# Kernel tuning notes

Hardware: AMD Instinct MI355X
Metric: run time of the kernel (lower is better)

The kernel has to match this reference:

```python
import jax, jax.numpy as jnp
import numpy as np

H, DH = 8, 64          # heads, dim_head
SCALE = DH ** -0.5

def _ln(x, g, b, eps=1e-5):
    m = jnp.mean(x, axis=-1, keepdims=True)
    v = jnp.var(x, axis=-1, keepdims=True)
    return (x - m) / jnp.sqrt(v + eps) * g + b

def setup_inputs() -> dict:
    key = jax.random.key(0)
    ks = jax.random.split(key, 16)
    b, n, din, dim, depth, mlp, nc = 4, 2048, 768, 512, 2, 512, 2
    s = 0.02
    x = jax.random.normal(ks[0], (b, n, din), jnp.float32)
    lens = jax.random.randint(ks[1], (b,), n // 2, n + 1)
    lens = lens.at[0].set(n)  # ensure amax(lens) == n so torch's truncation is a no-op
    return {
        "x": x,
        "lens": lens,
        "cls_token": jax.random.normal(ks[2], (1, 1, dim), jnp.float32),
        "fc_w": jax.random.normal(ks[3], (din, dim), jnp.float32) * s,
        "fc_b": jnp.zeros((dim,), jnp.float32),
        "ln1_g": jnp.ones((depth, dim), jnp.float32),
        "ln1_b": jnp.zeros((depth, dim), jnp.float32),
        "qkv_w": jax.random.normal(ks[4], (depth, dim, 3 * H * DH), jnp.float32) * s,
        "out_w": jax.random.normal(ks[5], (depth, H * DH, dim), jnp.float32) * s,
        "out_b": jnp.zeros((depth, dim), jnp.float32),
        "ln2_g": jnp.ones((depth, dim), jnp.float32),
        "ln2_b": jnp.zeros((depth, dim), jnp.float32),
        "ff1_w": jax.random.normal(ks[6], (depth, dim, mlp), jnp.float32) * s,
        "ff1_b": jnp.zeros((depth, mlp), jnp.float32),
        "ff2_w": jax.random.normal(ks[7], (depth, mlp, dim), jnp.float32) * s,
        "ff2_b": jnp.zeros((depth, dim), jnp.float32),
        "lnf_g": jnp.ones((dim,), jnp.float32),
        "lnf_b": jnp.zeros((dim,), jnp.float32),
        "head_w": jax.random.normal(ks[8], (dim, nc), jnp.float32) * s,
        "head_b": jnp.zeros((nc,), jnp.float32),
    }

def reference(x, lens, cls_token, fc_w, fc_b, ln1_g, ln1_b, qkv_w, out_w, out_b,
              ln2_g, ln2_b, ff1_w, ff1_b, ff2_w, ff2_b, lnf_g, lnf_b, head_w, head_b):
    b, n, _ = x.shape
    # fc + GELU (exact erf gelu, matching torch nn.GELU default)
    x = jax.nn.gelu(x @ fc_w + fc_b, approximate=False)
    x = jnp.concatenate([jnp.broadcast_to(cls_token, (b, 1, x.shape[-1])), x], axis=1)
    n1 = n + 1
    lens1 = lens + 1
    # faithful mask: mask @ mask.mT -> True only where BOTH query and key are padding
    pad = jnp.arange(n1)[None, :] >= lens1[:, None]           # [b, n1]
    mask2 = pad[:, :, None] & pad[:, None, :]                  # [b, n1, n1]
    neg = -jnp.finfo(x.dtype).max
    depth = qkv_w.shape[0]
    for l in range(depth):
        xn = _ln(x, ln1_g[l], ln1_b[l])
        qkv = xn @ qkv_w[l]                                    # [b, n1, 3*H*DH]
        q, k, v = jnp.split(qkv, 3, axis=-1)
        q = q.reshape(b, n1, H, DH).transpose(0, 2, 1, 3)      # [b, h, n1, dh]
        k = k.reshape(b, n1, H, DH).transpose(0, 2, 1, 3)
        v = v.reshape(b, n1, H, DH).transpose(0, 2, 1, 3)
        dots = jnp.einsum('bhid,bhjd->bhij', q, k) * SCALE
        dots = jnp.where(mask2[:, None], neg, dots)
        dots = dots - jnp.max(dots, axis=-1, keepdims=True)
        attn = jax.nn.softmax(dots, axis=-1)
        o = jnp.einsum('bhij,bhjd->bhid', attn, v)
        o = o.transpose(0, 2, 1, 3).reshape(b, n1, H * DH)
        x = o @ out_w[l] + out_b[l] + x
        h = jax.nn.gelu(_ln(x, ln2_g[l], ln2_b[l]) @ ff1_w[l] + ff1_b[l], approximate=False)
        x = h @ ff2_w[l] + ff2_b[l] + x
    x = _ln(x, lnf_g, lnf_b)
    return x[:, 0] @ head_w + head_b   # pool='cls'
```

## Files before the change

kernel.cpp:

```cpp
#include <hip/hip_runtime.h>
#include <hip/hip_bf16.h>
#include <math.h>
#include <float.h>

typedef __hip_bfloat16 bf16;
using bf16x8 = __attribute__((ext_vector_type(8))) __bf16;
using f32x4  = __attribute__((ext_vector_type(4))) float;

constexpr int BATCH = 4;
constexpr int SEQ   = 2048;
constexpr int SEQ1  = 2049;
constexpr int DIN   = 768;
constexpr int DIMC  = 512;
constexpr int DEPTH = 2;
constexpr int NHEAD = 8;
constexpr int DHEAD = 64;
constexpr int ROWS  = BATCH * SEQ1;
constexpr int VKP   = 2112;
constexpr float ATT_SCALE = 0.125f;
constexpr float NEGBIG = -1e30f;

__device__ __forceinline__ bf16x8 ld_frag(const bf16* p) { return *(const bf16x8*)p; }

__device__ __forceinline__ void g2lds16(const bf16* g, bf16* l) {
    __builtin_amdgcn_global_load_lds(
        (const __attribute__((address_space(1))) void*)g,
        (__attribute__((address_space(3))) void*)l, 16, 0, 0);
}

__global__ __launch_bounds__(256) void cast_kernel(const float* __restrict__ src,
                                                   bf16* __restrict__ dst, int n4) {
    int i = blockIdx.x * 256 + threadIdx.x;
    if (i < n4) {
        float4 v = ((const float4*)src)[i];
        dst[i * 4 + 0] = __float2bfloat16(v.x);
        dst[i * 4 + 1] = __float2bfloat16(v.y);
        dst[i * 4 + 2] = __float2bfloat16(v.z);
        dst[i * 4 + 3] = __float2bfloat16(v.w);
    }
}

__global__ __launch_bounds__(256) void wt_transpose_kernel(
    const float* __restrict__ src, bf16* __restrict__ dst,
    int R, int C, long zstride) {
    __shared__ bf16 tile[32][33];
    int z = blockIdx.z;
    const float* s = src + (size_t)z * zstride;
    bf16* d = dst + (size_t)z * zstride;
    int tx = threadIdx.x, ty = threadIdx.y;
    int c0 = blockIdx.x * 32, r0 = blockIdx.y * 32;
    int c = c0 + tx;
#pragma unroll
    for (int rr = ty; rr < 32; rr += 8) {
        int r = r0 + rr;
        tile[rr][tx] = (r < R && c < C) ? __float2bfloat16(s[(size_t)r * C + c])
                                        : __float2bfloat16(0.f);
    }
    __syncthreads();
    int rc = r0 + tx;
#pragma unroll
    for (int cc = ty; cc < 32; cc += 8) {
        int oc = c0 + cc;
        if (rc < R && oc < C) d[(size_t)oc * R + rc] = tile[tx][cc];
    }
}

__global__ __launch_bounds__(256) void vt_transpose_kernel(
    const bf16* __restrict__ QKV, bf16* __restrict__ VT) {
    __shared__ bf16 tile[32][33];
    int z = blockIdx.z;
    int bb = z >> 3, hh = z & 7;
    const bf16* s = QKV + (size_t)bb * SEQ1 * 1536 + 1024 + hh * 64;
    bf16* d = VT + (size_t)z * 64 * VKP;
    int tx = threadIdx.x, ty = threadIdx.y;
    int c0 = blockIdx.x * 32, r0 = blockIdx.y * 32;
    int c = c0 + tx;
#pragma unroll
    for (int rr = ty; rr < 32; rr += 8) {
        int r = r0 + rr;
        tile[rr][tx] = (r < SEQ1) ? s[(size_t)r * 1536 + c] : __float2bfloat16(0.f);
    }
    __syncthreads();
    int rc = r0 + tx;
#pragma unroll
    for (int cc = ty; cc < 32; cc += 8) {
        int oc = c0 + cc;
        if (rc < VKP) d[(size_t)oc * VKP + rc] = tile[tx][cc];
    }
}

__global__ void cls_fill_kernel(const float* __restrict__ cls, float* __restrict__ X) {
    int b = blockIdx.x;
    for (int d = threadIdx.x; d < DIMC; d += blockDim.x)
        X[(size_t)b * SEQ1 * DIMC + d] = cls[d];
}

template<int BM, bool GELU_, bool RESID, bool REMAP, bool OBF>
__global__ __launch_bounds__(256) void gemm_bt(
    const bf16* __restrict__ A, const bf16* __restrict__ Bt,
    const float* __restrict__ bias, const float* __restrict__ resid,
    float* __restrict__ Cf, bf16* __restrict__ Ch, int M, int N, int K) {
    constexpr int MI = BM / 32;
    __shared__ __align__(16) bf16 As[BM * 32];
    __shared__ __align__(16) bf16 Bs[4096];
    int tid = threadIdx.x;
    int ln = tid & 63, wv = tid >> 6;
    int wr = wv >> 1, wc = wv & 1;
    int l15 = ln & 15, l4 = ln >> 4;
    int m0 = blockIdx.y * BM, n0 = blockIdx.x * 128;

    f32x4 acc[MI][4];
#pragma unroll
    for (int i = 0; i < MI; ++i)
#pragma unroll
        for (int j = 0; j < 4; ++j) acc[i][j] = {0.f, 0.f, 0.f, 0.f};

    int aslot[MI], bslot[4];
#pragma unroll
    for (int i = 0; i < MI; ++i) {
        int m = wr * (BM / 2) + i * 16 + l15;
        aslot[i] = m * 4 + (l4 ^ ((m >> 1) & 3));
    }
#pragma unroll
    for (int j = 0; j < 4; ++j) {
        int n = wc * 64 + j * 16 + l15;
        bslot[j] = n * 4 + (l4 ^ ((n >> 1) & 3));
    }

    for (int k0 = 0; k0 < K; k0 += 32) {
#pragma unroll
        for (int r = 0; r < BM / 64; ++r) {
            int s = r * 256 + tid;
            int m = s >> 2, c = s & 3;
            int kb = c ^ ((m >> 1) & 3);
            int gm = m0 + m; if (gm > M - 1) gm = M - 1;
            g2lds16(A + (size_t)gm * K + k0 + kb * 8, &As[s * 8]);
        }
#pragma unroll
        for (int r = 0; r < 2; ++r) {
            int s = r * 256 + tid;
            int n = s >> 2, c = s & 3;
            int kb = c ^ ((n >> 1) & 3);
            g2lds16(Bt + (size_t)(n0 + n) * K + k0 + kb * 8, &Bs[s * 8]);
        }
        __syncthreads();
        bf16x8 af[MI], bfr[4];
#pragma unroll
        for (int i = 0; i < MI; ++i) af[i] = ld_frag(&As[aslot[i] * 8]);
#pragma unroll
        for (int j = 0; j < 4; ++j) bfr[j] = ld_frag(&Bs[bslot[j] * 8]);
#pragma unroll
        for (int i = 0; i < MI; ++i)
#pragma unroll
            for (int j = 0; j < 4; ++j)
                acc[i][j] = __builtin_amdgcn_mfma_f32_16x16x32_bf16(af[i], bfr[j], acc[i][j], 0, 0, 0);
        __syncthreads();
    }

#pragma unroll
    for (int i = 0; i < MI; ++i) {
#pragma unroll
        for (int j = 0; j < 4; ++j) {
            int gn = n0 + wc * 64 + j * 16 + l15;
            float bb = bias ? bias[gn] : 0.f;
#pragma unroll
            for (int r = 0; r < 4; ++r) {
                int gm = m0 + wr * (BM / 2) + i * 16 + l4 * 4 + r;
                if (gm >= M) continue;
                float v = acc[i][j][r] + bb;
                if (GELU_) v = 0.5f * v * (1.f + erff(v * 0.70710678118654752f));
                size_t orow = gm;
                if (REMAP) { int b_ = gm >> 11; orow = (size_t)b_ * SEQ1 + (gm & 2047) + 1; }
                size_t oi = orow * (size_t)N + gn;
                if (RESID) v += resid[oi];
                if (OBF) Ch[oi] = __float2bfloat16(v); else Cf[oi] = v;
            }
        }
    }
}

__global__ __launch_bounds__(256) void ln_kernel(const float* __restrict__ Xin, bf16* __restrict__ Xout,
                          const float* __restrict__ g, const float* __restrict__ bb) {
    int row = blockIdx.x;
    int t = threadIdx.x;
    const float* xr = Xin + (size_t)row * DIMC;
    float v0 = xr[t], v1 = xr[t + 256];
    __shared__ float red[256];
    red[t] = v0 + v1;
    __syncthreads();
    for (int w = 128; w > 0; w >>= 1) { if (t < w) red[t] += red[t + w]; __syncthreads(); }
    float mean = red[0] * (1.f / 512.f);
    __syncthreads();
    float d0 = v0 - mean, d1 = v1 - mean;
    red[t] = d0 * d0 + d1 * d1;
    __syncthreads();
    for (int w = 128; w > 0; w >>= 1) { if (t < w) red[t] += red[t + w]; __syncthreads(); }
    float rinv = rsqrtf(red[0] * (1.f / 512.f) + 1e-5f);
    bf16* orow = Xout + (size_t)row * DIMC;
    orow[t]       = __float2bfloat16(d0 * rinv * g[t]       + bb[t]);
    orow[t + 256] = __float2bfloat16(d1 * rinv * g[t + 256] + bb[t + 256]);
}

__global__ __launch_bounds__(256, 4) void attn_kernel(
    const bf16* __restrict__ QKV, const bf16* __restrict__ VT,
    const int* __restrict__ lens, bf16* __restrict__ O) {
    constexpr int KS = 72;
    __shared__ __align__(16) bf16 Ks[2][64 * KS];
    __shared__ __align__(16) bf16 Vs[2][64 * KS];
    int tid = threadIdx.x, ln = tid & 63, wv = tid >> 6;
    int l15 = ln & 15, l4 = ln >> 4;
    int q0 = blockIdx.x * 64, h = blockIdx.y, b = blockIdx.z;
    int len1 = lens[b] + 1;
    const bf16* qkv_b = QKV + (size_t)b * SEQ1 * 1536;
    const bf16* vt_b  = VT + (size_t)(b * 8 + h) * 64 * VKP;

    uint4 z4 = make_uint4(0u, 0u, 0u, 0u);
    uint4 q0v = z4, q1v = z4;
    int qrow = q0 + wv * 16 + l15;
    if (qrow < SEQ1) {
        const bf16* qp = qkv_b + (size_t)qrow * 1536 + h * 64 + l4 * 8;
        q0v = *(const uint4*)qp;
        q1v = *(const uint4*)(qp + 32);
    }
    bf16x8 bq0 = __builtin_bit_cast(bf16x8, q0v);
    bf16x8 bq1 = __builtin_bit_cast(bf16x8, q1v);
    bool qpad = (qrow >= len1);

    float mrun = NEGBIG, lrun = 0.f;
    f32x4 oaccT[4];
#pragma unroll
    for (int t = 0; t < 4; ++t) oaccT[t] = {0.f, 0.f, 0.f, 0.f};

    uint4 kr[2], vr[2];
    int srow[2], sseg[2], krow[2];
#pragma unroll
    for (int rr = 0; rr < 2; ++rr) {
        int idx = rr * 256 + tid;
        int row = idx >> 3, seg = idx & 7;
        srow[rr] = row; sseg[rr] = seg;
        int pb = row >> 5, w = row & 31;
        krow[rr] = pb * 32 + ((w >> 2) & 1) * 16 + (w >> 3) * 4 + (w & 3);
    }

#pragma unroll
    for (int rr = 0; rr < 2; ++rr) {
        kr[rr] = (srow[rr] < SEQ1)
            ? *(const uint4*)(qkv_b + (size_t)srow[rr] * 1536 + 512 + h * 64 + sseg[rr] * 8) : z4;
        vr[rr] = *(const uint4*)(vt_b + (size_t)srow[rr] * VKP + sseg[rr] * 8);
    }
#pragma unroll
    for (int rr = 0; rr < 2; ++rr) {
        *(uint4*)&Ks[0][krow[rr] * KS + sseg[rr] * 8] = kr[rr];
        *(uint4*)&Vs[0][srow[rr] * KS + sseg[rr] * 8] = vr[rr];
    }
    __syncthreads();

    for (int kt = 0; kt < 33; ++kt) {
        int k0 = kt * 64;
        int buf = kt & 1;
        if (kt < 32) {
            int kn = k0 + 64;
#pragma unroll
            for (int rr = 0; rr < 2; ++rr) {
                kr[rr] = (kn + srow[rr] < SEQ1)
                    ? *(const uint4*)(qkv_b + (size_t)(kn + srow[rr]) * 1536 + 512 + h * 64 + sseg[rr] * 8) : z4;
                vr[rr] = *(const uint4*)(vt_b + (size_t)srow[rr] * VKP + kn + sseg[rr] * 8);
            }
        }

        f32x4 sacc[2][2];
#pragma unroll
        for (int pb = 0; pb < 2; ++pb)
#pragma unroll
            for (int s = 0; s < 2; ++s) {
                int R = pb * 32 + s * 16 + l15;
                f32x4 a = {0.f, 0.f, 0.f, 0.f};
                bf16x8 kf0 = ld_frag(&Ks[buf][R * KS + l4 * 8]);
                bf16x8 kf1 = ld_frag(&Ks[buf][R * KS + 32 + l4 * 8]);
                a = __builtin_amdgcn_mfma_f32_16x16x32_bf16(kf0, bq0, a, 0, 0, 0);
                a = __builtin_amdgcn_mfma_f32_16x16x32_bf16(kf1, bq1, a, 0, 0, 0);
                sacc[pb][s] = a;
            }

        float sv[2][2][4];
        float mx = NEGBIG;
#pragma unroll
        for (int pb = 0; pb < 2; ++pb)
#pragma unroll
            for (int s = 0; s < 2; ++s)
#pragma unroll
                for (int r = 0; r < 4; ++r) {
                    int j = k0 + pb * 32 + l4 * 8 + s * 4 + r;
                    float v = sacc[pb][s][r] * ATT_SCALE;
                    if (j >= SEQ1 || (qpad && j >= len1)) v = NEGBIG;
                    sv[pb][s][r] = v;
                    mx = fmaxf(mx, v);
                }
        mx = fmaxf(mx, __shfl_xor(mx, 16, 64));
        mx = fmaxf(mx, __shfl_xor(mx, 32, 64));
        float mnew = fmaxf(mrun, mx);
        float alpha = __expf(mrun - mnew);
        float rs = 0.f;
        unsigned short pk[2][8];
#pragma unroll
        for (int pb = 0; pb < 2; ++pb)
#pragma unroll
            for (int s = 0; s < 2; ++s)
#pragma unroll
                for (int r = 0; r < 4; ++r) {
                    float ex = sv[pb][s][r] - mnew;
                    float p = (ex < -80.f) ? 0.f : __expf(ex);
                    rs += p;
                    pk[pb][s * 4 + r] = __builtin_bit_cast(unsigned short, __float2bfloat16(p));
                }
        rs += __shfl_xor(rs, 16, 64);
        rs += __shfl_xor(rs, 32, 64);
        lrun = lrun * alpha + rs;
        mrun = mnew;
#pragma unroll
        for (int t = 0; t < 4; ++t) {
            oaccT[t][0] *= alpha; oaccT[t][1] *= alpha;
            oaccT[t][2] *= alpha; oaccT[t][3] *= alpha;
        }

#pragma unroll
        for (int pb = 0; pb < 2; ++pb) {
            union { unsigned short u[8]; bf16x8 v; } pu;
#pragma unroll
            for (int e = 0; e < 8; ++e) pu.u[e] = pk[pb][e];
            bf16x8 pf = pu.v;
#pragma unroll
            for (int t = 0; t < 4; ++t) {
                bf16x8 vf = ld_frag(&Vs[buf][(t * 16 + l15) * KS + pb * 32 + l4 * 8]);
                oaccT[t] = __builtin_amdgcn_mfma_f32_16x16x32_bf16(vf, pf, oaccT[t], 0, 0, 0);
            }
        }

        if (kt < 32) {
            int ob = buf ^ 1;
#pragma unroll
            for (int rr = 0; rr < 2; ++rr) {
                *(uint4*)&Ks[ob][krow[rr] * KS + sseg[rr] * 8] = kr[rr];
                *(uint4*)&Vs[ob][srow[rr] * KS + sseg[rr] * 8] = vr[rr];
            }
        }
        __syncthreads();
    }

    if (qrow < SEQ1) {
        float rl = (lrun > 0.f) ? 1.f / lrun : 0.f;
        bf16* orow = O + ((size_t)b * SEQ1 + qrow) * DIMC + h * 64;
#pragma unroll
        for (int t = 0; t < 4; ++t) {
            union { unsigned short u[4]; uint2 v; } ou;
#pragma unroll
            for (int r = 0; r < 4; ++r)
                ou.u[r] = __builtin_bit_cast(unsigned short, __float2bfloat16(oaccT[t][r] * rl));
            *(uint2*)&orow[t * 16 + l4 * 4] = ou.v;
        }
    }
}

__global__ __launch_bounds__(256) void head_kernel(const float* __restrict__ X,
                            const float* __restrict__ g, const float* __restrict__ bb,
                            const float* __restrict__ hw, const float* __restrict__ hb,
                            float* __restrict__ out) {
    int b = blockIdx.x, t = threadIdx.x;
    const float* xr = X + (size_t)b * SEQ1 * DIMC;
    float v0 = xr[t], v1 = xr[t + 256];
    __shared__ float red[256];
    red[t] = v0 + v1;
    __syncthreads();
    for (int w = 128; w > 0; w >>= 1) { if (t < w) red[t] += red[t + w]; __syncthreads(); }
    float mean = red[0] * (1.f / 512.f);
    __syncthreads();
    float d0 = v0 - mean, d1 = v1 - mean;
    red[t] = d0 * d0 + d1 * d1;
    __syncthreads();
    for (int w = 128; w > 0; w >>= 1) { if (t < w) red[t] += red[t + w]; __syncthreads(); }
    float rinv = rsqrtf(red[0] * (1.f / 512.f) + 1e-5f);
    __syncthreads();
    float xn0 = d0 * rinv * g[t] + bb[t];
    float xn1 = d1 * rinv * g[t + 256] + bb[t + 256];
    float p0 = xn0 * hw[t * 2]     + xn1 * hw[(t + 256) * 2];
    float p1 = xn0 * hw[t * 2 + 1] + xn1 * hw[(t + 256) * 2 + 1];
    __shared__ float r0[256], r1[256];
    r0[t] = p0; r1[t] = p1;
    __syncthreads();
    for (int w = 128; w > 0; w >>= 1) { if (t < w) { r0[t] += r0[t + w]; r1[t] += r1[t + w]; } __syncthreads(); }
    if (t == 0) {
        out[b * 2 + 0] = r0[0] + hb[0];
        out[b * 2 + 1] = r1[0] + hb[1];
    }
}

extern "C" void kernel_launch(void* const* d_in, const int* in_sizes, int n_in,
                              void* d_out, int out_size, void* d_ws, size_t ws_size,
                              hipStream_t stream) {
    const float* x      = (const float*)d_in[0];
    const int*   lens   = (const int*)d_in[1];
    const float* cls    = (const float*)d_in[2];
    const float* fc_w   = (const float*)d_in[3];
    const float* fc_b   = (const float*)d_in[4];
    const float* ln1_g  = (const float*)d_in[5];
    const float* ln1_b  = (const float*)d_in[6];
    const float* qkv_w  = (const float*)d_in[7];
    const float* out_w  = (const float*)d_in[8];
    const float* out_b  = (const float*)d_in[9];
    const float* ln2_g  = (const float*)d_in[10];
    const float* ln2_b  = (const float*)d_in[11];
    const float* ff1_w  = (const float*)d_in[12];
    const float* ff1_b  = (const float*)d_in[13];
    const float* ff2_w  = (const float*)d_in[14];
    const float* ff2_b  = (const float*)d_in[15];
    const float* lnf_g  = (const float*)d_in[16];
    const float* lnf_b  = (const float*)d_in[17];
    const float* head_w = (const float*)d_in[18];
    const float* head_b = (const float*)d_in[19];
    float* out = (float*)d_out;

    char* w = (char*)d_ws;
    float* X    = (float*)w;  w += (size_t)ROWS * DIMC * 4;
    bf16*  XNh  = (bf16*)w;   w += (size_t)ROWS * DIMC * 2;
    bf16*  QKVh = (bf16*)w;   w += (size_t)ROWS * 1536 * 2;
    bf16*  Obh  = (bf16*)w;   w += (size_t)ROWS * DIMC * 2;
    bf16*  xbf  = (bf16*)w;   w += (size_t)BATCH * SEQ * DIN * 2;
    bf16*  VT   = xbf;
    bf16*  fc_wt  = (bf16*)w;
    bf16*  qkv_wt = fc_wt  + (size_t)DIN * DIMC;
    bf16*  out_wt = qkv_wt + (size_t)2 * DIMC * 1536;
    bf16*  ff1_wt = out_wt + (size_t)2 * DIMC * DIMC;
    bf16*  ff2_wt = ff1_wt + (size_t)2 * DIMC * DIMC;
    bf16*  Hbh  = Obh;

    dim3 blk(256);
    dim3 tb(32, 8);

    cast_kernel<<<dim3((BATCH * SEQ * DIN / 4 + 255) / 256), blk, 0, stream>>>(
        x, xbf, BATCH * SEQ * DIN / 4);

    wt_transpose_kernel<<<dim3(16, 24, 1), tb, 0, stream>>>(fc_w,  fc_wt,  DIN,  DIMC, (long)DIN * DIMC);
    wt_transpose_kernel<<<dim3(48, 16, 2), tb, 0, stream>>>(qkv_w, qkv_wt, DIMC, 1536, (long)DIMC * 1536);
    wt_transpose_kernel<<<dim3(16, 16, 2), tb, 0, stream>>>(out_w, out_wt, DIMC, DIMC, (long)DIMC * DIMC);
    wt_transpose_kernel<<<dim3(16, 16, 2), tb, 0, stream>>>(ff1_w, ff1_wt, DIMC, DIMC, (long)DIMC * DIMC);
    wt_transpose_kernel<<<dim3(16, 16, 2), tb, 0, stream>>>(ff2_w, ff2_wt, DIMC, DIMC, (long)DIMC * DIMC);

    gemm_bt<64, true, false, true, false><<<dim3(4, 128), blk, 0, stream>>>(
        xbf, fc_wt, fc_b, nullptr, X, nullptr, BATCH * SEQ, DIMC, DIN);
    cls_fill_kernel<<<dim3(BATCH), blk, 0, stream>>>(cls, X);

    for (int l = 0; l < DEPTH; ++l) {
        ln_kernel<<<dim3(ROWS), blk, 0, stream>>>(X, XNh, ln1_g + l * DIMC, ln1_b + l * DIMC);
        gemm_bt<128, false, false, false, true><<<dim3(12, 65), blk, 0, stream>>>(
            XNh, qkv_wt + (size_t)l * DIMC * 1536, nullptr, nullptr, nullptr, QKVh, ROWS, 1536, DIMC);
        vt_transpose_kernel<<<dim3(2, 66, 32), tb, 0, stream>>>(QKVh, VT);
        attn_kernel<<<dim3(33, NHEAD, BATCH), blk, 0, stream>>>(QKVh, VT, lens, Obh);
        gemm_bt<64, false, true, false, false><<<dim3(4, 129), blk, 0, stream>>>(
            Obh, out_wt + (size_t)l * DIMC * DIMC, out_b + l * DIMC, X, X, nullptr, ROWS, DIMC, DIMC);
        ln_kernel<<<dim3(ROWS), blk, 0, stream>>>(X, XNh, ln2_g + l * DIMC, ln2_b + l * DIMC);
        gemm_bt<64, true, false, false, true><<<dim3(4, 129), blk, 0, stream>>>(
            XNh, ff1_wt + (size_t)l * DIMC * DIMC, ff1_b + l * DIMC, nullptr, nullptr, Hbh, ROWS, DIMC, DIMC);
        gemm_bt<64, false, true, false, false><<<dim3(4, 129), blk, 0, stream>>>(
            Hbh, ff2_wt + (size_t)l * DIMC * DIMC, ff2_b + l * DIMC, X, X, nullptr, ROWS, DIMC, DIMC);
    }
    head_kernel<<<dim3(BATCH), blk, 0, stream>>>(X, lnf_g, lnf_b, head_w, head_b, out);
}
```

Baseline: 619.4 us.

## Warp-per-row LayerNorm, XOR-swizzled attention LDS, skip unneeded masking

LayerNorm now gives each row to one 64-lane wavefront with vectorized float4 loads and shuffle reductions, replacing the block-wide shared-memory tree reduction and its many barriers. The attention kernel drops the padded LDS rows in favour of an XOR-swizzled 16-byte-slot layout for K and V. The smaller footprint allows launch bounds to rise to 5 blocks per CU. Per-element masking is also skipped for key tiles that lie entirely inside the valid length. The swizzle must stay consistent between writes and fragment reads, and the higher occupancy target may constrain registers.

```diff
diff --git a/kernel.cpp b/kernel.cpp
--- a/kernel.cpp
+++ b/kernel.cpp
@@ -181,32 +181,42 @@
 
 __global__ __launch_bounds__(256) void ln_kernel(const float* __restrict__ Xin, bf16* __restrict__ Xout,
                           const float* __restrict__ g, const float* __restrict__ bb) {
-    int row = blockIdx.x;
-    int t = threadIdx.x;
-    const float* xr = Xin + (size_t)row * DIMC;
-    float v0 = xr[t], v1 = xr[t + 256];
-    __shared__ float red[256];
-    red[t] = v0 + v1;
-    __syncthreads();
-    for (int w = 128; w > 0; w >>= 1) { if (t < w) red[t] += red[t + w]; __syncthreads(); }
-    float mean = red[0] * (1.f / 512.f);
-    __syncthreads();
-    float d0 = v0 - mean, d1 = v1 - mean;
-    red[t] = d0 * d0 + d1 * d1;
-    __syncthreads();
-    for (int w = 128; w > 0; w >>= 1) { if (t < w) red[t] += red[t + w]; __syncthreads(); }
-    float rinv = rsqrtf(red[0] * (1.f / 512.f) + 1e-5f);
-    bf16* orow = Xout + (size_t)row * DIMC;
-    orow[t]       = __float2bfloat16(d0 * rinv * g[t]       + bb[t]);
-    orow[t + 256] = __float2bfloat16(d1 * rinv * g[t + 256] + bb[t + 256]);
-}
-
-__global__ __launch_bounds__(256, 4) void attn_kernel(
+    int wv = threadIdx.x >> 6, ln = threadIdx.x & 63;
+    int row = blockIdx.x * 4 + wv;
+    if (row >= ROWS) return;
+    const float* xr = Xin + (size_t)row * DIMC + ln * 8;
+    float4 a = *(const float4*)xr;
+    float4 c = *(const float4*)(xr + 4);
+    float s = a.x + a.y + a.z + a.w + c.x + c.y + c.z + c.w;
+#pragma unroll
+    for (int off = 1; off < 64; off <<= 1) s += __shfl_xor(s, off, 64);
+    float mean = s * (1.f / 512.f);
+    float d[8] = {a.x - mean, a.y - mean, a.z - mean, a.w - mean,
+                  c.x - mean, c.y - mean, c.z - mean, c.w - mean};
+    float var = 0.f;
+#pragma unroll
+    for (int e = 0; e < 8; ++e) var += d[e] * d[e];
+#pragma unroll
+    for (int off = 1; off < 64; off <<= 1) var += __shfl_xor(var, off, 64);
+    float rinv = rsqrtf(var * (1.f / 512.f) + 1e-5f);
+    const float* gp = g + ln * 8;
+    const float* bp = bb + ln * 8;
+    float4 g0 = *(const float4*)gp, g1 = *(const float4*)(gp + 4);
+    float4 b0 = *(const float4*)bp, b1 = *(const float4*)(bp + 4);
+    float gg[8] = {g0.x, g0.y, g0.z, g0.w, g1.x, g1.y, g1.z, g1.w};
+    float bbv[8] = {b0.x, b0.y, b0.z, b0.w, b1.x, b1.y, b1.z, b1.w};
+    union { unsigned short u[8]; uint4 v; } ou;
+#pragma unroll
+    for (int e = 0; e < 8; ++e)
+        ou.u[e] = __builtin_bit_cast(unsigned short, __float2bfloat16(d[e] * rinv * gg[e] + bbv[e]));
+    *(uint4*)(Xout + (size_t)row * DIMC + ln * 8) = ou.v;
+}
+
+__global__ __launch_bounds__(256, 5) void attn_kernel(
     const bf16* __restrict__ QKV, const bf16* __restrict__ VT,
     const int* __restrict__ lens, bf16* __restrict__ O) {
-    constexpr int KS = 72;
-    __shared__ __align__(16) bf16 Ks[2][64 * KS];
-    __shared__ __align__(16) bf16 Vs[2][64 * KS];
+    __shared__ __align__(16) bf16 Ks[2][4096];
+    __shared__ __align__(16) bf16 Vs[2][4096];
     int tid = threadIdx.x, ln = tid & 63, wv = tid >> 6;
     int l15 = ln & 15, l4 = ln >> 4;
     int q0 = blockIdx.x * 64, h = blockIdx.y, b = blockIdx.z;
@@ -232,14 +242,17 @@
     for (int t = 0; t < 4; ++t) oaccT[t] = {0.f, 0.f, 0.f, 0.f};
 
     uint4 kr[2], vr[2];
-    int srow[2], sseg[2], krow[2];
+    int srow[2], sseg[2];
+    int kslot[2], vslot[2];
 #pragma unroll
     for (int rr = 0; rr < 2; ++rr) {
         int idx = rr * 256 + tid;
         int row = idx >> 3, seg = idx & 7;
         srow[rr] = row; sseg[rr] = seg;
         int pb = row >> 5, w = row & 31;
-        krow[rr] = pb * 32 + ((w >> 2) & 1) * 16 + (w >> 3) * 4 + (w & 3);
+        int krow = pb * 32 + ((w >> 2) & 1) * 16 + (w >> 3) * 4 + (w & 3);
+        kslot[rr] = krow * 8 + (seg ^ (krow & 7));
+        vslot[rr] = row * 8 + (seg ^ (row & 7));
     }
 
 #pragma unroll
@@ -250,8 +263,8 @@
     }
 #pragma unroll
     for (int rr = 0; rr < 2; ++rr) {
-        *(uint4*)&Ks[0][krow[rr] * KS + sseg[rr] * 8] = kr[rr];
-        *(uint4*)&Vs[0][srow[rr] * KS + sseg[rr] * 8] = vr[rr];
+        *(uint4*)&Ks[0][kslot[rr] * 8] = kr[rr];
+        *(uint4*)&Vs[0][vslot[rr] * 8] = vr[rr];
     }
     __syncthreads();
 
@@ -275,13 +288,14 @@
             for (int s = 0; s < 2; ++s) {
                 int R = pb * 32 + s * 16 + l15;
                 f32x4 a = {0.f, 0.f, 0.f, 0.f};
-                bf16x8 kf0 = ld_frag(&Ks[buf][R * KS + l4 * 8]);
-                bf16x8 kf1 = ld_frag(&Ks[buf][R * KS + 32 + l4 * 8]);
+                bf16x8 kf0 = ld_frag(&Ks[buf][(R * 8 + (l4 ^ (R & 7))) * 8]);
+                bf16x8 kf1 = ld_frag(&Ks[buf][(R * 8 + ((l4 + 4) ^ (R & 7))) * 8]);
                 a = __builtin_amdgcn_mfma_f32_16x16x32_bf16(kf0, bq0, a, 0, 0, 0);
                 a = __builtin_amdgcn_mfma_f32_16x16x32_bf16(kf1, bq1, a, 0, 0, 0);
                 sacc[pb][s] = a;
             }
 
+        bool needmask = (k0 + 64 > len1) || (kt == 32);
         float sv[2][2][4];
         float mx = NEGBIG;
 #pragma unroll
@@ -290,9 +304,11 @@
             for (int s = 0; s < 2; ++s)
 #pragma unroll
                 for (int r = 0; r < 4; ++r) {
-                    int j = k0 + pb * 32 + l4 * 8 + s * 4 + r;
                     float v = sacc[pb][s][r] * ATT_SCALE;
-                    if (j >= SEQ1 || (qpad && j >= len1)) v = NEGBIG;
+                    if (needmask) {
+                        int j = k0 + pb * 32 + l4 * 8 + s * 4 + r;
+                        if (j >= SEQ1 || (qpad && j >= len1)) v = NEGBIG;
+                    }
                     sv[pb][s][r] = v;
                     mx = fmaxf(mx, v);
                 }
@@ -331,7 +347,8 @@
             bf16x8 pf = pu.v;
 #pragma unroll
             for (int t = 0; t < 4; ++t) {
-                bf16x8 vf = ld_frag(&Vs[buf][(t * 16 + l15) * KS + pb * 32 + l4 * 8]);
+                int VR = t * 16 + l15;
+                bf16x8 vf = ld_frag(&Vs[buf][(VR * 8 + ((pb * 4 + l4) ^ (VR & 7))) * 8]);
                 oaccT[t] = __builtin_amdgcn_mfma_f32_16x16x32_bf16(vf, pf, oaccT[t], 0, 0, 0);
             }
         }
@@ -340,8 +357,8 @@
             int ob = buf ^ 1;
 #pragma unroll
             for (int rr = 0; rr < 2; ++rr) {
-                *(uint4*)&Ks[ob][krow[rr] * KS + sseg[rr] * 8] = kr[rr];
-                *(uint4*)&Vs[ob][srow[rr] * KS + sseg[rr] * 8] = vr[rr];
+                *(uint4*)&Ks[ob][kslot[rr] * 8] = kr[rr];
+                *(uint4*)&Vs[ob][vslot[rr] * 8] = vr[rr];
             }
         }
         __syncthreads();
@@ -450,14 +467,14 @@
     cls_fill_kernel<<<dim3(BATCH), blk, 0, stream>>>(cls, X);
 
     for (int l = 0; l < DEPTH; ++l) {
-        ln_kernel<<<dim3(ROWS), blk, 0, stream>>>(X, XNh, ln1_g + l * DIMC, ln1_b + l * DIMC);
+        ln_kernel<<<dim3((ROWS + 3) / 4), blk, 0, stream>>>(X, XNh, ln1_g + l * DIMC, ln1_b + l * DIMC);
         gemm_bt<128, false, false, false, true><<<dim3(12, 65), blk, 0, stream>>>(
             XNh, qkv_wt + (size_t)l * DIMC * 1536, nullptr, nullptr, nullptr, QKVh, ROWS, 1536, DIMC);
         vt_transpose_kernel<<<dim3(2, 66, 32), tb, 0, stream>>>(QKVh, VT);
         attn_kernel<<<dim3(33, NHEAD, BATCH), blk, 0, stream>>>(QKVh, VT, lens, Obh);
         gemm_bt<64, false, true, false, false><<<dim3(4, 129), blk, 0, stream>>>(
             Obh, out_wt + (size_t)l * DIMC * DIMC, out_b + l * DIMC, X, X, nullptr, ROWS, DIMC, DIMC);
-        ln_kernel<<<dim3(ROWS), blk, 0, stream>>>(X, XNh, ln2_g + l * DIMC, ln2_b + l * DIMC);
+        ln_kernel<<<dim3((ROWS + 3) / 4), blk, 0, stream>>>(X, XNh, ln2_g + l * DIMC, ln2_b + l * DIMC);
         gemm_bt<64, true, false, false, true><<<dim3(4, 129), blk, 0, stream>>>(
             XNh, ff1_wt + (size_t)l * DIMC * DIMC, ff1_b + l * DIMC, nullptr, nullptr, Hbh, ROWS, DIMC, DIMC);
         gemm_bt<64, false, true, false, false><<<dim3(4, 129), blk, 0, stream>>>(
```

Result: faster. 588.8 us (-4.9%).
